# Kernel tuning notes

Hardware: AMD Instinct MI355X
Metric: run time of the kernel (lower is better)

Reference implementation:

```python
import jax, jax.numpy as jnp
import numpy as np

B, N, STEPS = 256, 2048, 64
DT = 0.1  # integration step size


def setup_inputs() -> dict:
    key = jax.random.key(0)
    ks = jax.random.split(key, 7)
    lim = 1.0 / np.sqrt(N)            # torch Linear default init bound
    kstd = np.sqrt(2.0) * np.sqrt(2.0 / N)  # custom kaiming_init std (gain*sqrt(2/size))
    return {
        "x0": jax.random.normal(ks[0], (B, N), dtype=jnp.float32),
        "free_inds": jnp.ones((B, N), dtype=jnp.float32),
        "W_w": jax.random.uniform(ks[1], (N, N), jnp.float32, -lim, lim),
        "W_b": jax.random.uniform(ks[2], (N,), jnp.float32, -lim, lim),
        "T_w": jax.random.uniform(ks[3], (N, N), jnp.float32, -lim, lim),
        "T_b": jax.random.uniform(ks[4], (N,), jnp.float32, -lim, lim),
        "w_proc_to_syn": jax.random.normal(ks[5], (N,), jnp.float32) * kstd,
        "w_syn_to_proc": jax.random.normal(ks[6], (N,), jnp.float32) * kstd,
    }


def reference(x0, free_inds, W_w, W_b, T_w, T_b, w_proc_to_syn, w_syn_to_proc):
    # Faithful to the torch forward: s0/p0 are ignored, x = s = p = x0.
    def step(carry, _):
        x, s, p = carry
        phi = jax.nn.relu(x)   # processing activation
        g = jax.nn.relu(s)     # synaptic gate
        psi = jax.nn.relu(p)   # plasticity activation
        dx = -x + (g * phi) @ W_w.T + W_b
        ds = -s + w_proc_to_syn * psi + phi
        dp = -p + psi @ T_w.T + T_b + w_syn_to_proc * g
        x_n = x + DT * dx * free_inds
        s_n = p + DT * ds   # note: s update uses p as the base, as in the source
        p_n = p + DT * dp
        return (x_n, s_n, p_n), x_n

    (x, s, p), xs = jax.lax.scan(step, (x0, x0, x0), None, length=STEPS)
    return x, xs  # xs: [STEPS, B, N]
```

## Files before the change

### kernel.cpp

```cpp
#include <hip/hip_runtime.h>
#include <hip/hip_bf16.h>

#define BB 256
#define NN 2048
#define NSTEPS 64
#define DT_C 0.1f
#define WSCALE 512.0f
#define ASCALE 8.0f
#define ACC_INV (1.0f / 4096.0f)

#define SLOT (1u << 20)
#define PSOFF (1u << 19)

typedef __attribute__((ext_vector_type(4))) float floatx4;
typedef __attribute__((ext_vector_type(4))) float f32x4;

__device__ __forceinline__ floatx4 mfma_fp8(long long a, long long b, floatx4 c) {
  return __builtin_amdgcn_mfma_f32_16x16x32_fp8_fp8(a, b, c, 0, 0, 0);
}

__device__ __forceinline__ unsigned pack4_fp8(float a, float b, float c, float d) {
  int lo = __builtin_amdgcn_cvt_pk_fp8_f32(a, b, 0, false);
  int r  = __builtin_amdgcn_cvt_pk_fp8_f32(c, d, lo, true);
  return (unsigned)r;
}
__device__ __forceinline__ unsigned char fp8byte(float v) {
  return (unsigned char)(__builtin_amdgcn_cvt_pk_fp8_f32(v, 0.f, 0, false) & 0xff);
}

__device__ __forceinline__ long long sysload(const long long* p) {
  return __hip_atomic_load(p, __ATOMIC_RELAXED, __HIP_MEMORY_SCOPE_SYSTEM);
}
__device__ __forceinline__ void sysstore(unsigned* p, unsigned v) {
  __hip_atomic_store(p, v, __ATOMIC_RELAXED, __HIP_MEMORY_SCOPE_SYSTEM);
}
template <bool C>
__device__ __forceinline__ long long aload(const long long* p) {
  if constexpr (C) return *p;
  else return sysload(p);
}


__global__ __launch_bounds__(256) void convert_kernel(
    const float* __restrict__ Ww, unsigned char* __restrict__ Wf,
    const float* __restrict__ Tw, unsigned char* __restrict__ Tf, int half) {
  int bid = blockIdx.x;
  const float* src = Ww;
  unsigned char* dst = Wf;
  if (bid >= half) { bid -= half; src = Tw; dst = Tf; }
  const int g = bid * 256 + threadIdx.x;
  const int frag = g >> 6, l = g & 63;
  const int j = (frag >> 6) * 16 + (l & 15);
  const int k = (frag & 63) * 32 + (l >> 4) * 8;
  const float* s = src + (size_t)j * NN + k;
  unsigned lo = pack4_fp8(s[0] * WSCALE, s[1] * WSCALE, s[2] * WSCALE, s[3] * WSCALE);
  unsigned hi = pack4_fp8(s[4] * WSCALE, s[5] * WSCALE, s[6] * WSCALE, s[7] * WSCALE);
  ((unsigned long long*)dst)[g] = ((unsigned long long)hi << 32) | lo;
}

__global__ __launch_bounds__(256) void init_kernel(
    const float* __restrict__ x0, unsigned char* __restrict__ Ab) {
  const int i = blockIdx.x * 256 + threadIdx.x;
  const int b = i >> 11, j = i & (NN - 1);
  const float r = fmaxf(x0[i], 0.f);
  const int dl = (b & 15) | (((j >> 3) & 3) << 4);
  const size_t fo = ((size_t)((b >> 4) * 64 + (j >> 5))) * 512 + dl * 8 + (j & 7);
  Ab[fo] = fp8byte(ASCALE * r * r);
  Ab[PSOFF + fo] = fp8byte(ASCALE * r);
}

#define LOADA(S, kc) \
  S##a0 = aload<CACHED>(aP0 + (size_t)(kc) * 64); \
  S##a1 = aload<CACHED>(aP1 + (size_t)(kc) * 64);
#define LOADB(S, kc) \
  S##b0 = bP0[(size_t)(kc) * 64]; \
  S##b1 = bP1[(size_t)(kc) * 64]; \
  S##b2 = bP2[(size_t)(kc) * 64]; \
  S##b3 = bP3[(size_t)(kc) * 64];
#define DOMFMA(S) \
  acc00 = mfma_fp8(S##a0, S##b0, acc00); acc01 = mfma_fp8(S##a0, S##b1, acc01); \
  acc02 = mfma_fp8(S##a0, S##b2, acc02); acc03 = mfma_fp8(S##a0, S##b3, acc03); \
  acc10 = mfma_fp8(S##a1, S##b0, acc10); acc11 = mfma_fp8(S##a1, S##b1, acc11); \
  acc12 = mfma_fp8(S##a1, S##b2, acc12); acc13 = mfma_fp8(S##a1, S##b3, acc13);

template <bool CACHED>
__global__ __launch_bounds__(512) void fused_kernel(
    const unsigned char* __restrict__ Wf, const unsigned char* __restrict__ Tf,
    const float* __restrict__ Wb, const float* __restrict__ Tb,
    const float* __restrict__ wp2s, const float* __restrict__ ws2p,
    const float* __restrict__ fri, const float* __restrict__ x0,
    unsigned char* __restrict__ Ab,
    float* __restrict__ out, unsigned* __restrict__ bar) {
  __shared__ float eb[8][32][68];

  if constexpr (CACHED)
    __builtin_amdgcn_fence(__ATOMIC_ACQUIRE, "agent");

  const int tid = threadIdx.x;
  const int lane = tid & 63, wv = tid >> 6;
  const int lane15 = lane & 15, kq = lane >> 4;
  const int g = wv >> 2, h = wv & 3;

  const int x = blockIdx.x & 7, ii = blockIdx.x >> 3;
  const int colt = x * 4 + (ii & 3), rowt = ii >> 2;
  const int b0 = rowt * 32, j0 = colt * 64;

  const int erow = tid >> 4;
  const int c4 = (tid & 15) << 2;
  const int ej = j0 + c4;
  const size_t eidx = (size_t)(b0 + erow) * NN + ej;
  const f32x4 Wb4 = *(const f32x4*)(Wb + ej);
  const f32x4 Tb4 = *(const f32x4*)(Tb + ej);
  const f32x4 wp4 = *(const f32x4*)(wp2s + ej);
  const f32x4 ws4 = *(const f32x4*)(ws2p + ej);
  const f32x4 fr4 = *(const f32x4*)(fri + eidx);
  f32x4 xcur = *(const f32x4*)(x0 + eidx);
  f32x4 scur = xcur, pcur = xcur;

  const int bb = b0 + erow;
  const int dl = (bb & 15) | (((ej >> 3) & 3) << 4);
  const size_t fob = ((size_t)((bb >> 4) * 64 + (ej >> 5))) * 512 + dl * 8 + (ej & 7);

  const int rf0 = rowt * 2;
  const int cf0 = colt * 4;
  const int kcb = h * 16;
  const unsigned char* Bfm = g == 0 ? Wf : Tf;
  const long long* bP0 = (const long long*)Bfm + ((size_t)(cf0 + 0) * 64 + kcb) * 64 + lane;
  const long long* bP1 = (const long long*)Bfm + ((size_t)(cf0 + 1) * 64 + kcb) * 64 + lane;
  const long long* bP2 = (const long long*)Bfm + ((size_t)(cf0 + 2) * 64 + kcb) * 64 + lane;
  const long long* bP3 = (const long long*)Bfm + ((size_t)(cf0 + 3) * 64 + kcb) * 64 + lane;
  const size_t aOff0 = ((size_t)(rf0 + 0) * 64 + kcb) * 64 + lane;
  const size_t aOff1 = ((size_t)(rf0 + 1) * 64 + kcb) * 64 + lane;

  float* xs = out + (size_t)BB * NN;

  long long Aa0, Aa1, Ab0, Ab1, Ab2, Ab3;
  long long Ba0, Ba1, Bb0, Bb1, Bb2, Bb3;
  long long Ca0, Ca1, Cb0, Cb1, Cb2, Cb3;
  long long Da0, Da1, Db0, Db1, Db2, Db3;
  LOADB(A, 0) LOADB(B, 1) LOADB(C, 2) LOADB(D, 3)

  for (int t = 0; t < NSTEPS; ++t) {
    const unsigned rs  = CACHED ? (unsigned)t : (unsigned)(t & 1);
    const unsigned wsl = CACHED ? (unsigned)(t + 1) : (unsigned)((t + 1) & 1);
    const unsigned char* Ar = Ab + (size_t)rs * SLOT + (g == 0 ? 0u : PSOFF);
    unsigned char* Uw  = Ab + (size_t)wsl * SLOT;
    unsigned char* PSw = Uw + PSOFF;
    const long long* aP0 = (const long long*)Ar + aOff0;
    const long long* aP1 = (const long long*)Ar + aOff1;

    LOADA(A, 0) LOADA(B, 1) LOADA(C, 2) LOADA(D, 3)

    floatx4 acc00 = {0.f,0.f,0.f,0.f}, acc01 = {0.f,0.f,0.f,0.f};
    floatx4 acc02 = {0.f,0.f,0.f,0.f}, acc03 = {0.f,0.f,0.f,0.f};
    floatx4 acc10 = {0.f,0.f,0.f,0.f}, acc11 = {0.f,0.f,0.f,0.f};
    floatx4 acc12 = {0.f,0.f,0.f,0.f}, acc13 = {0.f,0.f,0.f,0.f};

    for (int kc = 0; kc < 12; kc += 4) {
      DOMFMA(A) LOADA(A, kc + 4) LOADB(A, kc + 4)
      DOMFMA(B) LOADA(B, kc + 5) LOADB(B, kc + 5)
      DOMFMA(C) LOADA(C, kc + 6) LOADB(C, kc + 6)
      DOMFMA(D) LOADA(D, kc + 7) LOADB(D, kc + 7)
    }
    DOMFMA(A) LOADB(A, 0)
    DOMFMA(B) LOADB(B, 1)
    DOMFMA(C) LOADB(C, 2)
    DOMFMA(D) LOADB(D, 3)

#pragma unroll
    for (int r = 0; r < 4; ++r) {
      eb[wv][kq * 4 + r][lane15]      = acc00[r];
      eb[wv][kq * 4 + r][16 + lane15] = acc01[r];
      eb[wv][kq * 4 + r][32 + lane15] = acc02[r];
      eb[wv][kq * 4 + r][48 + lane15] = acc03[r];
      eb[wv][16 + kq * 4 + r][lane15]      = acc10[r];
      eb[wv][16 + kq * 4 + r][16 + lane15] = acc11[r];
      eb[wv][16 + kq * 4 + r][32 + lane15] = acc12[r];
      eb[wv][16 + kq * 4 + r][48 + lane15] = acc13[r];
    }
    __syncthreads();

    f32x4 m1, m2;
    {
      const f32x4 p0 = *(const f32x4*)&eb[0][erow][c4];
      const f32x4 p1 = *(const f32x4*)&eb[1][erow][c4];
      const f32x4 p2 = *(const f32x4*)&eb[2][erow][c4];
      const f32x4 p3 = *(const f32x4*)&eb[3][erow][c4];
      const f32x4 q0 = *(const f32x4*)&eb[4][erow][c4];
      const f32x4 q1 = *(const f32x4*)&eb[5][erow][c4];
      const f32x4 q2 = *(const f32x4*)&eb[6][erow][c4];
      const f32x4 q3 = *(const f32x4*)&eb[7][erow][c4];
      m1 = ((p0 + p1) + (p2 + p3)) * ACC_INV;
      m2 = ((q0 + q1) + (q2 + q3)) * ACC_INV;
    }
    float uf[4], pf[4];
#pragma unroll
    for (int e = 0; e < 4; ++e) {
      const float xv = xcur[e], s = scur[e], p = pcur[e];
      const float phi = fmaxf(xv, 0.f), gg = fmaxf(s, 0.f), psi = fmaxf(p, 0.f);
      const float xn = xv + DT_C * (-xv + m1[e] + Wb4[e]) * fr4[e];
      const float sn = p + DT_C * (-s + wp4[e] * psi + phi);
      const float pn = p + DT_C * (-p + m2[e] + Tb4[e] + ws4[e] * gg);
      xcur[e] = xn; scur[e] = sn; pcur[e] = pn;
      uf[e] = ASCALE * fmaxf(xn, 0.f) * fmaxf(sn, 0.f);
      pf[e] = ASCALE * fmaxf(pn, 0.f);
    }
    if (t == NSTEPS - 1) {
      __builtin_nontemporal_store(xcur, (f32x4*)(xs + (size_t)t * BB * NN + eidx));
      __builtin_nontemporal_store(xcur, (f32x4*)(out + eidx));
    } else {
      sysstore((unsigned*)(Uw + fob), pack4_fp8(uf[0], uf[1], uf[2], uf[3]));
      sysstore((unsigned*)(PSw + fob), pack4_fp8(pf[0], pf[1], pf[2], pf[3]));
      asm volatile("s_waitcnt vmcnt(0)" ::: "memory");
      __syncthreads();
      __builtin_nontemporal_store(xcur,
          (f32x4*)(xs + (size_t)t * BB * NN + eidx));
      if (tid == 0) {
        unsigned* leaf = bar + 32 * (1 + x);
        const unsigned v = __hip_atomic_fetch_add(leaf, 1u, __ATOMIC_RELAXED,
                                                  __HIP_MEMORY_SCOPE_AGENT);
        if (v + 1 == 32u * (unsigned)(t + 1))
          __hip_atomic_fetch_add(bar, 1u, __ATOMIC_RELAXED, __HIP_MEMORY_SCOPE_AGENT);
        while (__hip_atomic_load(bar, __ATOMIC_RELAXED, __HIP_MEMORY_SCOPE_AGENT)
               < 8u * (unsigned)(t + 1))
          __builtin_amdgcn_s_sleep(1);
      }
      __syncthreads();
    }
  }
}

extern "C" void kernel_launch(void* const* d_in, const int* in_sizes, int n_in,
                              void* d_out, int out_size, void* d_ws, size_t ws_size,
                              hipStream_t stream) {
  const float* x0   = (const float*)d_in[0];
  const float* fri  = (const float*)d_in[1];
  const float* Ww   = (const float*)d_in[2];
  const float* Wb   = (const float*)d_in[3];
  const float* Tw   = (const float*)d_in[4];
  const float* Tb   = (const float*)d_in[5];
  const float* wp2s = (const float*)d_in[6];
  const float* ws2p = (const float*)d_in[7];
  float* out = (float*)d_out;

  const size_t BN = (size_t)BB * NN;
  const size_t NW = (size_t)NN * NN;

  const size_t needCached = 4096 + 64 * (size_t)SLOT + 2 * NW;
  const bool cached = ws_size >= needCached;
  const size_t nslots = cached ? 64 : 2;

  unsigned* bar = (unsigned*)d_ws;
  unsigned char* Abuf = (unsigned char*)d_ws + 4096;
  unsigned char* Wf = Abuf + nslots * (size_t)SLOT;
  unsigned char* Tf = Wf + NW;

  hipMemsetAsync(bar, 0, 4096, stream);
  const int chalf = (int)(NW / 2048);
  convert_kernel<<<2 * chalf, 256, 0, stream>>>(Ww, Wf, Tw, Tf, chalf);
  init_kernel<<<(int)(BN / 256), 256, 0, stream>>>(x0, Abuf);

  void* kargs[] = {
    (void*)&Wf, (void*)&Tf, (void*)&Wb, (void*)&Tb, (void*)&wp2s, (void*)&ws2p,
    (void*)&fri, (void*)&x0, (void*)&Abuf, (void*)&out, (void*)&bar
  };
  if (cached) {
    hipLaunchCooperativeKernel((const void*)fused_kernel<true>, dim3(256),
                               dim3(512), kargs, 0, stream);
  } else {
    hipLaunchCooperativeKernel((const void*)fused_kernel<false>, dim3(256),
                               dim3(512), kargs, 0, stream);
  }
}
```

Before: 458.8 us.

## Replace global grid barrier with per-dependency step flags in cached path

In the cached path, each block now publishes a per-block step counter after writing its fp8 activations, instead of joining a two-level atomic grid barrier. Before loading its A operands, each wave polls only the eight flags of the blocks that produce the rows and k-chunks it needs. This removes the all-to-all barrier and lets blocks move ahead as soon as their own inputs are ready. The non-cached path keeps the tree barrier, relocated to bar+256. The risk is correctness if the flag indexing misses a producer, or if the relaxed system-scope atomics do not order the data writes before the flag store.

```diff
diff --git a/kernel.cpp b/kernel.cpp
--- a/kernel.cpp
+++ b/kernel.cpp
@@ -29,6 +29,9 @@
 }
 
 __device__ __forceinline__ long long sysload(const long long* p) {
+  return __hip_atomic_load(p, __ATOMIC_RELAXED, __HIP_MEMORY_SCOPE_SYSTEM);
+}
+__device__ __forceinline__ unsigned sysloadu(const unsigned* p) {
   return __hip_atomic_load(p, __ATOMIC_RELAXED, __HIP_MEMORY_SCOPE_SYSTEM);
 }
 __device__ __forceinline__ void sysstore(unsigned* p, unsigned v) {
@@ -132,6 +135,8 @@
   const size_t aOff0 = ((size_t)(rf0 + 0) * 64 + kcb) * 64 + lane;
   const size_t aOff1 = ((size_t)(rf0 + 1) * 64 + kcb) * 64 + lane;
 
+  const unsigned* myflags = bar + rowt * 32 + 8 * h + (lane & 7);
+
   float* xs = out + (size_t)BB * NN;
 
   long long Aa0, Aa1, Ab0, Ab1, Ab2, Ab3;
@@ -148,6 +153,17 @@
     unsigned char* PSw = Uw + PSOFF;
     const long long* aP0 = (const long long*)Ar + aOff0;
     const long long* aP1 = (const long long*)Ar + aOff1;
+
+    if (CACHED && t > 0) {
+      for (;;) {
+        int ok = 1;
+        if ((lane & 63) < 8) ok = (sysloadu(myflags) >= (unsigned)t) ? 1 : 0;
+        if (__all(ok)) break;
+        __builtin_amdgcn_s_sleep(1);
+      }
+      asm volatile("" ::: "memory");
+      __builtin_amdgcn_sched_barrier(0);
+    }
 
     LOADA(A, 0) LOADA(B, 1) LOADA(C, 2) LOADA(D, 3)
 
@@ -213,19 +229,28 @@
       sysstore((unsigned*)(PSw + fob), pack4_fp8(pf[0], pf[1], pf[2], pf[3]));
       asm volatile("s_waitcnt vmcnt(0)" ::: "memory");
       __syncthreads();
-      __builtin_nontemporal_store(xcur,
-          (f32x4*)(xs + (size_t)t * BB * NN + eidx));
-      if (tid == 0) {
-        unsigned* leaf = bar + 32 * (1 + x);
-        const unsigned v = __hip_atomic_fetch_add(leaf, 1u, __ATOMIC_RELAXED,
-                                                  __HIP_MEMORY_SCOPE_AGENT);
-        if (v + 1 == 32u * (unsigned)(t + 1))
-          __hip_atomic_fetch_add(bar, 1u, __ATOMIC_RELAXED, __HIP_MEMORY_SCOPE_AGENT);
-        while (__hip_atomic_load(bar, __ATOMIC_RELAXED, __HIP_MEMORY_SCOPE_AGENT)
-               < 8u * (unsigned)(t + 1))
-          __builtin_amdgcn_s_sleep(1);
+      if constexpr (CACHED) {
+        if (tid == 0)
+          sysstore(bar + rowt * 32 + colt, (unsigned)(t + 1));
+        __builtin_nontemporal_store(xcur,
+            (f32x4*)(xs + (size_t)t * BB * NN + eidx));
+      } else {
+        __builtin_nontemporal_store(xcur,
+            (f32x4*)(xs + (size_t)t * BB * NN + eidx));
+        if (tid == 0) {
+          unsigned* root = bar + 256;
+          unsigned* leaf = root + 32 * (1 + x);
+          const unsigned v = __hip_atomic_fetch_add(leaf, 1u, __ATOMIC_RELAXED,
+                                                    __HIP_MEMORY_SCOPE_AGENT);
+          if (v + 1 == 32u * (unsigned)(t + 1))
+            __hip_atomic_fetch_add(root, 1u, __ATOMIC_RELAXED,
+                                   __HIP_MEMORY_SCOPE_AGENT);
+          while (__hip_atomic_load(root, __ATOMIC_RELAXED,
+                                   __HIP_MEMORY_SCOPE_AGENT) < 8u * (unsigned)(t + 1))
+            __builtin_amdgcn_s_sleep(1);
+        }
+        __syncthreads();
       }
-      __syncthreads();
     }
   }
 }
```

New measurement: 599.8 us. 30.7% more time.
